# Kernel optimization log

Hardware: AMD Instinct MI355X
Metric: run time of the kernel (lower is better)

## Reference

```python
import jax, jax.numpy as jnp
import numpy as np

NUM_SAMPLES = 64
NUM_FINE_SAMPLES = 128
BATCH = 131072


def setup_inputs() -> dict:
    key = jax.random.key(0)
    k1, k2, k3, k4 = jax.random.split(key, 4)
    near = 0.5 + jax.random.uniform(k1, (BATCH, 1), dtype=jnp.float32)          # [0.5, 1.5]
    far = near + 2.0 + 4.0 * jax.random.uniform(k2, (BATCH, 1), dtype=jnp.float32)  # near + [2, 6]
    density = 5.0 * jax.random.uniform(k3, (BATCH, NUM_SAMPLES), dtype=jnp.float32)
    rgb = jax.random.uniform(k4, (BATCH, NUM_SAMPLES, 3), dtype=jnp.float32)
    return {"near": near, "far": far, "density": density, "rgb": rgb}


def _hierarchical_sample(bins, weights, num_samples):
    # bins, weights: [B, N]; deterministic u (pertube=False branch)
    B, N = weights.shape
    pdf = weights / (jnp.sum(weights, -1, keepdims=True) + 1e-6)
    cdf = jnp.cumsum(pdf, -1)                                   # [B, N]
    u = jnp.broadcast_to(jnp.linspace(0.05, 0.95, num_samples, dtype=bins.dtype), (B, num_samples))
    inds = jax.vmap(lambda c, uu: jnp.searchsorted(c, uu, side='right'))(cdf, u)  # [B, Nf]
    below = jnp.maximum(inds - 1, 0)
    above = jnp.minimum(inds, N - 1)
    cdf_b = jnp.take_along_axis(cdf, below, -1)
    cdf_a = jnp.take_along_axis(cdf, above, -1)
    bins_b = jnp.take_along_axis(bins, below, -1)
    bins_a = jnp.take_along_axis(bins, above, -1)
    denom = cdf_a - cdf_b
    denom = jnp.where(denom < 1e-5, jnp.ones_like(denom), denom)
    t = (u - cdf_b) / denom
    return bins_b + t * (bins_a - bins_b)                       # [B, Nf]


def reference(near, far, density, rgb):
    # --- coarse frustum (deterministic, pertub=False path of _sample_coarse_frustum) ---
    unit = jnp.linspace(0.0, 1.0, NUM_SAMPLES + 1, dtype=near.dtype)  # [N+1]
    zs_edges = near * (1.0 - unit) + far * unit                 # [B, N+1]
    start, end = zs_edges[:, :-1], zs_edges[:, 1:]
    deltas = end - start                                        # [B, N]
    mids = 0.5 * (start + end)                                  # frustum.zs, [B, N]

    # --- _compute_weight: alpha compositing transmittance ---
    alpha = 1.0 - jnp.exp(-density * deltas)                    # [B, N]
    trans = jnp.cumprod(jnp.concatenate([jnp.ones_like(alpha[:, :1]), 1.0 - alpha], -1), -1)[:, :-1]
    weight = alpha * trans                                      # [B, N]

    # --- _sample_fine_frustum: inverse-CDF sampling + merge-sort of zs ---
    fine_zs = _hierarchical_sample(mids, weight, NUM_FINE_SAMPLES)  # [B, Nf] (no_grad in original)
    fine_zs = jax.lax.stop_gradient(fine_zs)
    combined_zs = jnp.sort(jnp.concatenate([mids, fine_zs], -1), -1)  # [B, N+Nf]

    # --- volume_render of the coarse pass ---
    rgb_out = jnp.sum(weight[..., None] * rgb, axis=1)          # [B, 3]
    acc = jnp.sum(weight, -1, keepdims=True)                    # [B, 1]
    depth = jnp.sum(weight * mids, -1, keepdims=True) / (acc + 1e-8)  # normalized composite
    return combined_zs, rgb_out, depth, acc
```

## Files before the change

kernel.cpp:

```cpp
#include <hip/hip_runtime.h>

#define BATCH 131072
#define NS 64
#define NF 128
#define NTOT 192
#define WPB 4

__global__ __launch_bounds__(256) void pdf_sampler_kernel(
    const float* __restrict__ near_p,
    const float* __restrict__ far_p,
    const float* __restrict__ density,
    const float* __restrict__ rgb,
    float* __restrict__ out)
{
    const int lane = threadIdx.x & 63;
    const int wave = threadIdx.x >> 6;
    const int ray  = blockIdx.x * WPB + wave;

    __shared__ float2 s_cm  [WPB][NS];
    __shared__ int    s_inds[WPB][NF];
    __shared__ __align__(16) float s_comb[WPB][NTOT];

    const float nearv = near_p[ray];
    const float farv  = far_p[ray];

    const float u0 = (float)lane       * (1.0f / 64.0f);
    const float u1 = (float)(lane + 1) * (1.0f / 64.0f);
    const float zs = nearv * (1.0f - u0) + farv * u0;
    const float ze = nearv * (1.0f - u1) + farv * u1;
    const float delta = ze - zs;
    const float mid   = 0.5f * (zs + ze);

    const float dens = density[ray * NS + lane];

    float S = dens * delta;
    #pragma unroll
    for (int off = 1; off < 64; off <<= 1) {
        float t = __shfl_up(S, off, 64);
        if (lane >= off) S += t;
    }
    const float e = expf(-S);
    float eprev = __shfl_up(e, 1, 64);
    if (lane == 0) eprev = 1.0f;
    const float w = eprev - e;

    const float wsum = 1.0f - __shfl(e, 63, 64);
    const float cdfv = (1.0f - e) * __builtin_amdgcn_rcpf(wsum + 1e-6f);

    s_cm[wave][lane] = make_float2(cdfv, mid);

    const float step = 0.9f / 127.0f;
    int t = (int)ceilf((cdfv - 0.05f) * (127.0f / 0.9f));
    t = t < 0 ? 0 : (t > 128 ? 128 : t);
    while (t > 0   && __fmaf_rn(step, (float)(t - 1), 0.05f) >= cdfv) --t;
    while (t < 128 && __fmaf_rn(step, (float)t,       0.05f) <  cdfv) ++t;

    int t1 = __shfl_down(t, 1, 64);
    if (lane == 63) t1 = 128;
    const int t0 = __shfl(t, 0, 64);

    for (int k = lane; k < t0; k += 64) s_inds[wave][k] = 0;
    for (int k = t; k < t1; ++k) s_inds[wave][k] = lane + 1;

    const float r = rgb[(ray * NS + lane) * 3 + 0];
    const float g = rgb[(ray * NS + lane) * 3 + 1];
    const float b = rgb[(ray * NS + lane) * 3 + 2];
    float wr = w * r, wg = w * g, wb = w * b, wm = w * mid;
    #pragma unroll
    for (int off = 32; off; off >>= 1) {
        wr += __shfl_xor(wr, off, 64);
        wg += __shfl_xor(wg, off, 64);
        wb += __shfl_xor(wb, off, 64);
        wm += __shfl_xor(wm, off, 64);
    }
    if (lane == 0) {
        float* rgb_out   = out + (size_t)BATCH * NTOT;
        float* depth_out = rgb_out + (size_t)BATCH * 3;
        float* acc_out   = depth_out + BATCH;
        rgb_out[ray * 3 + 0] = wr;
        rgb_out[ray * 3 + 1] = wg;
        rgb_out[ray * 3 + 2] = wb;
        depth_out[ray] = wm / (wsum + 1e-8f);
        acc_out[ray]   = wsum;
    }

    __syncthreads();

    #pragma unroll
    for (int i = 0; i < 2; ++i) {
        const int k = lane + 64 * i;
        const int inds  = s_inds[wave][k];
        const int below = inds > 0 ? inds - 1 : 0;
        const int above = inds < 63 ? inds : 63;
        const float2 cb2 = s_cm[wave][below];
        const float2 ca2 = s_cm[wave][above];
        float denom = ca2.x - cb2.x;
        if (denom < 1e-5f) denom = 1.0f;
        const float u  = __fmaf_rn(step, (float)k, 0.05f);
        const float tt = (u - cb2.x) * __builtin_amdgcn_rcpf(denom);
        const float fine = cb2.y + tt * (ca2.y - cb2.y);
        s_comb[wave][k + below + 1] = fine;
    }
    const int pm = (lane == 0) ? 0 : lane + t;
    s_comb[wave][pm] = mid;

    __syncthreads();

    float* comb_out = out + (size_t)ray * NTOT;
    if (lane < 48) {
        const float4 v = *reinterpret_cast<const float4*>(&s_comb[wave][lane * 4]);
        reinterpret_cast<float4*>(comb_out)[lane] = v;
    }
}

extern "C" void kernel_launch(void* const* d_in, const int* in_sizes, int n_in,
                              void* d_out, int out_size, void* d_ws, size_t ws_size,
                              hipStream_t stream) {
    const float* near_p  = (const float*)d_in[0];
    const float* far_p   = (const float*)d_in[1];
    const float* density = (const float*)d_in[2];
    const float* rgb     = (const float*)d_in[3];
    float* out = (float*)d_out;

    const int grid = BATCH / WPB;
    pdf_sampler_kernel<<<grid, 256, 0, stream>>>(near_p, far_p, density, rgb, out);
}
```

Before: 235.7 us.

## Use DPP wave scans, LDS histogram for sample indices, and drop block barriers

Replaces the shuffle-based prefix sum and reductions with DPP row/broadcast scans. The serial per-lane fill of the searchsorted index array becomes an LDS atomic histogram followed by a wave prefix scan. Global loads are hoisted to the top of the kernel. Block-wide __syncthreads are replaced by wave barriers because each wave owns one ray. This cuts instruction latency and removes divergent fill loops and cross-wave synchronisation, but it relies on wave-local LDS ordering and changes the exp to the fast __expf approximation.

Result: faster. 205.2 us (-12.9%).

```diff
diff --git a/kernel.cpp b/kernel.cpp
--- a/kernel.cpp
+++ b/kernel.cpp
@@ -5,6 +5,31 @@
 #define NF 128
 #define NTOT 192
 #define WPB 4
+
+#define DPP_ADD_F(x, ctrl, rm)                                               \
+    x += __int_as_float(__builtin_amdgcn_update_dpp(                         \
+        0, __float_as_int(x), ctrl, rm, 0xf, true))
+#define DPP_ADD_I(x, ctrl, rm)                                               \
+    x += __builtin_amdgcn_update_dpp(0, x, ctrl, rm, 0xf, true)
+
+__device__ __forceinline__ float wave_iscan_f(float x) {
+    DPP_ADD_F(x, 0x111, 0xf);
+    DPP_ADD_F(x, 0x112, 0xf);
+    DPP_ADD_F(x, 0x114, 0xf);
+    DPP_ADD_F(x, 0x118, 0xf);
+    DPP_ADD_F(x, 0x142, 0xa);
+    DPP_ADD_F(x, 0x143, 0xc);
+    return x;
+}
+__device__ __forceinline__ int wave_iscan_i(int x) {
+    DPP_ADD_I(x, 0x111, 0xf);
+    DPP_ADD_I(x, 0x112, 0xf);
+    DPP_ADD_I(x, 0x114, 0xf);
+    DPP_ADD_I(x, 0x118, 0xf);
+    DPP_ADD_I(x, 0x142, 0xa);
+    DPP_ADD_I(x, 0x143, 0xc);
+    return x;
+}
 
 __global__ __launch_bounds__(256) void pdf_sampler_kernel(
     const float* __restrict__ near_p,
@@ -17,12 +42,16 @@
     const int wave = threadIdx.x >> 6;
     const int ray  = blockIdx.x * WPB + wave;
 
-    __shared__ float2 s_cm  [WPB][NS];
-    __shared__ int    s_inds[WPB][NF];
+    __shared__ float2 s_cm[WPB][NS];
+    __shared__ int2   s_hist2[WPB][NF / 2];
     __shared__ __align__(16) float s_comb[WPB][NTOT];
 
     const float nearv = near_p[ray];
     const float farv  = far_p[ray];
+    const float dens  = density[ray * NS + lane];
+    const float r = rgb[(ray * NS + lane) * 3 + 0];
+    const float g = rgb[(ray * NS + lane) * 3 + 1];
+    const float b = rgb[(ray * NS + lane) * 3 + 2];
 
     const float u0 = (float)lane       * (1.0f / 64.0f);
     const float u1 = (float)(lane + 1) * (1.0f / 64.0f);
@@ -31,23 +60,16 @@
     const float delta = ze - zs;
     const float mid   = 0.5f * (zs + ze);
 
-    const float dens = density[ray * NS + lane];
-
-    float S = dens * delta;
-    #pragma unroll
-    for (int off = 1; off < 64; off <<= 1) {
-        float t = __shfl_up(S, off, 64);
-        if (lane >= off) S += t;
-    }
-    const float e = expf(-S);
-    float eprev = __shfl_up(e, 1, 64);
-    if (lane == 0) eprev = 1.0f;
-    const float w = eprev - e;
-
+    const float S = wave_iscan_f(dens * delta);
+    const float e = __expf(-S);
+    const float eprev = __int_as_float(__builtin_amdgcn_update_dpp(
+        0x3f800000, __float_as_int(e), 0x138, 0xf, 0xf, false));
+    const float w    = eprev - e;
     const float wsum = 1.0f - __shfl(e, 63, 64);
     const float cdfv = (1.0f - e) * __builtin_amdgcn_rcpf(wsum + 1e-6f);
 
     s_cm[wave][lane] = make_float2(cdfv, mid);
+    s_hist2[wave][lane] = make_int2(0, 0);
 
     const float step = 0.9f / 127.0f;
     int t = (int)ceilf((cdfv - 0.05f) * (127.0f / 0.9f));
@@ -55,56 +77,49 @@
     while (t > 0   && __fmaf_rn(step, (float)(t - 1), 0.05f) >= cdfv) --t;
     while (t < 128 && __fmaf_rn(step, (float)t,       0.05f) <  cdfv) ++t;
 
-    int t1 = __shfl_down(t, 1, 64);
-    if (lane == 63) t1 = 128;
-    const int t0 = __shfl(t, 0, 64);
+    __builtin_amdgcn_wave_barrier();
+    if (t < 128) atomicAdd(&((int*)s_hist2[wave])[t], 1);
+    __builtin_amdgcn_wave_barrier();
 
-    for (int k = lane; k < t0; k += 64) s_inds[wave][k] = 0;
-    for (int k = t; k < t1; ++k) s_inds[wave][k] = lane + 1;
+    const int2 h   = s_hist2[wave][lane];
+    const int incl = wave_iscan_i(h.x + h.y);
+    const int inds0 = incl - h.y;
+    const int inds1 = incl;
 
-    const float r = rgb[(ray * NS + lane) * 3 + 0];
-    const float g = rgb[(ray * NS + lane) * 3 + 1];
-    const float b = rgb[(ray * NS + lane) * 3 + 2];
-    float wr = w * r, wg = w * g, wb = w * b, wm = w * mid;
-    #pragma unroll
-    for (int off = 32; off; off >>= 1) {
-        wr += __shfl_xor(wr, off, 64);
-        wg += __shfl_xor(wg, off, 64);
-        wb += __shfl_xor(wb, off, 64);
-        wm += __shfl_xor(wm, off, 64);
-    }
-    if (lane == 0) {
+    const float wrS = wave_iscan_f(w * r);
+    const float wgS = wave_iscan_f(w * g);
+    const float wbS = wave_iscan_f(w * b);
+    const float wmS = wave_iscan_f(w * mid);
+    if (lane == 63) {
         float* rgb_out   = out + (size_t)BATCH * NTOT;
         float* depth_out = rgb_out + (size_t)BATCH * 3;
         float* acc_out   = depth_out + BATCH;
-        rgb_out[ray * 3 + 0] = wr;
-        rgb_out[ray * 3 + 1] = wg;
-        rgb_out[ray * 3 + 2] = wb;
-        depth_out[ray] = wm / (wsum + 1e-8f);
+        rgb_out[ray * 3 + 0] = wrS;
+        rgb_out[ray * 3 + 1] = wgS;
+        rgb_out[ray * 3 + 2] = wbS;
+        depth_out[ray] = wmS * __builtin_amdgcn_rcpf(wsum + 1e-8f);
         acc_out[ray]   = wsum;
     }
 
-    __syncthreads();
-
     #pragma unroll
     for (int i = 0; i < 2; ++i) {
-        const int k = lane + 64 * i;
-        const int inds  = s_inds[wave][k];
+        const int k    = 2 * lane + i;
+        const int inds = i ? inds1 : inds0;
         const int below = inds > 0 ? inds - 1 : 0;
-        const int above = inds < 63 ? inds : 63;
+        const int above = inds < NS - 1 ? inds : NS - 1;
         const float2 cb2 = s_cm[wave][below];
         const float2 ca2 = s_cm[wave][above];
         float denom = ca2.x - cb2.x;
         if (denom < 1e-5f) denom = 1.0f;
         const float u  = __fmaf_rn(step, (float)k, 0.05f);
         const float tt = (u - cb2.x) * __builtin_amdgcn_rcpf(denom);
-        const float fine = cb2.y + tt * (ca2.y - cb2.y);
+        const float fine = __fmaf_rn(tt, ca2.y - cb2.y, cb2.y);
         s_comb[wave][k + below + 1] = fine;
     }
-    const int pm = (lane == 0) ? 0 : lane + t;
+    const int pm = lane ? lane + t : 0;
     s_comb[wave][pm] = mid;
 
-    __syncthreads();
+    __builtin_amdgcn_wave_barrier();
 
     float* comb_out = out + (size_t)ray * NTOT;
     if (lane < 48) {
```
